# Optimization experiments

Hardware: AMD Instinct MI355X
Metric: run time of the kernel (lower is better)

## Reference

```python
import jax, jax.numpy as jnp
import numpy as np

# Mamba hyperparams (mamba_ssm defaults for d_model=128)
D_MODEL = 128
DEPTH = 8
D_INNER = 256   # expand=2
D_STATE = 16
D_CONV = 4
DT_RANK = 8     # ceil(D_MODEL/16)
EPS = 1e-5


def setup_inputs() -> dict:
    key = jax.random.key(0)
    ks = jax.random.split(key, 8)
    B, H, W = 1, 48, 48
    s = lambda k, shape, sc=0.02: jax.random.normal(k, shape, jnp.float32) * sc
    return {
        "x": jax.random.normal(ks[0], (B, D_MODEL, H, W), jnp.float32),
        "W_in": s(ks[1], (DEPTH, D_MODEL, 2 * D_INNER)),
        "conv_w": s(ks[2], (DEPTH, D_INNER, D_CONV), 0.2),
        "conv_b": jnp.zeros((DEPTH, D_INNER), jnp.float32),
        "W_xproj": s(ks[3], (DEPTH, D_INNER, DT_RANK + 2 * D_STATE)),
        "W_dt": s(ks[4], (DEPTH, DT_RANK, D_INNER), 0.1),
        "b_dt": jnp.full((DEPTH, D_INNER), -4.6, jnp.float32),  # softplus ~= 0.01
        "A_log": jnp.broadcast_to(
            jnp.log(jnp.arange(1, D_STATE + 1, dtype=jnp.float32)),
            (DEPTH, D_INNER, D_STATE)).copy(),
        "D_skip": jnp.ones((DEPTH, D_INNER), jnp.float32),
        "W_out": s(ks[5], (DEPTH, D_INNER, D_MODEL)),
        "rms_w": jnp.ones((DEPTH, D_MODEL), jnp.float32),
    }


def _rmsnorm(x, w):
    return x * jax.lax.rsqrt(jnp.mean(x * x, axis=-1, keepdims=True) + EPS) * w


def _mamba_layer(x, Wi, cw, cb, Wx, Wdt, bdt, Alog, Dp, Wo):
    # x: [B, L, D_MODEL]
    B, L, _ = x.shape
    xz = x @ Wi                                   # [B, L, 2*d_inner]
    xi, z = jnp.split(xz, 2, axis=-1)
    # causal depthwise conv1d, kernel D_CONV
    xp = jnp.pad(xi, ((0, 0), (D_CONV - 1, 0), (0, 0)))
    xc = sum(xp[:, k:k + L, :] * cw[:, k] for k in range(D_CONV)) + cb
    xc = jax.nn.silu(xc)                          # [B, L, d_inner]
    dbl = xc @ Wx                                 # [B, L, dt_rank + 2*d_state]
    dt_r = dbl[..., :DT_RANK]
    Bs = dbl[..., DT_RANK:DT_RANK + D_STATE]      # [B, L, d_state]
    Cs = dbl[..., DT_RANK + D_STATE:]
    dt = jax.nn.softplus(dt_r @ Wdt + bdt)        # [B, L, d_inner]
    A = -jnp.exp(Alog)                            # [d_inner, d_state]
    dA = jnp.exp(dt[..., None] * A)               # [B, L, d_inner, d_state]
    dBx = (dt * xc)[..., None] * Bs[:, :, None, :]
    # linear recurrence h_t = dA_t * h_{t-1} + dBx_t via parallel scan
    def comb(l, r):
        al, bl = l
        ar, br = r
        return ar * al, ar * bl + br
    _, h = jax.lax.associative_scan(comb, (dA, dBx), axis=1)
    y = jnp.einsum('blds,bls->bld', h, Cs) + Dp * xc
    y = y * jax.nn.silu(z)
    return y @ Wo                                 # [B, L, D_MODEL]


def reference(x, W_in, conv_w, conv_b, W_xproj, W_dt, b_dt, A_log, D_skip, W_out, rms_w):
    B, C, H, W = x.shape
    seq = x.reshape(B, C, H * W).transpose(0, 2, 1)  # [B, L, C]
    for l in range(DEPTH):
        seq = _mamba_layer(seq, W_in[l], conv_w[l], conv_b[l], W_xproj[l],
                           W_dt[l], b_dt[l], A_log[l], D_skip[l], W_out[l])
        seq = _rmsnorm(seq, rms_w[l])
    return seq.reshape(B, H, W, C).transpose(0, 3, 1, 2)
```

## Files before the change

kernel.cpp:

```cpp
#include <hip/hip_runtime.h>
#include <math.h>

#define LSEQ 2304
#define DM 128
#define DI 256
#define DS 16
#define RK 8
#define NCH 576
#define CLEN 4
#define NG 24
#define GS 24
#define NSI (DI*DS)
#define EPSF 1e-5f

__device__ __forceinline__ float silu_f(float s) { return s / (1.f + __expf(-s)); }
__device__ __forceinline__ float softplus_f(float x) { return (x > 20.f) ? x : log1pf(__expf(x)); }

template<bool FIRST>
__global__ __launch_bounds__(256, 4)
void k_in(const float* __restrict__ seq, const float* __restrict__ x0,
          const float* __restrict__ Wi,
          const float* __restrict__ cw, const float* __restrict__ cbias,
          float* __restrict__ xc_g, float* __restrict__ sz_g) {
    __shared__ float As[19 * 128];
    const int l0 = blockIdx.x * 16;
    const int half = blockIdx.y & 1;
    const bool isZ = blockIdx.y >= 2;
    const int tid = threadIdx.x;

    if (FIRST) {
        const int rlo = isZ ? 3 : 0;
        for (int idx = tid + rlo * 128; idx < 19 * 128; idx += 256) {
            const int r = idx >> 7, cc = idx & 127;
            const int l = l0 - 3 + r;
            As[idx] = (l >= 0) ? x0[cc * LSEQ + l] : 0.f;
        }
    } else if (!isZ) {
        for (int idx = tid; idx < 19 * 32; idx += 256) {
            const int r = idx >> 5, cq = (idx & 31) * 4;
            const int l = l0 - 3 + r;
            const float4 v = (l >= 0) ? *(const float4*)&seq[l * DM + cq]
                                      : make_float4(0.f, 0.f, 0.f, 0.f);
            *(float4*)&As[r * 128 + cq] = v;
        }
    } else {
        for (int idx = tid; idx < 16 * 32; idx += 256) {
            const int r = 3 + (idx >> 5), cq = (idx & 31) * 4;
            *(float4*)&As[r * 128 + cq] =
                *(const float4*)&seq[(l0 - 3 + r) * DM + cq];
        }
    }
    __syncthreads();

    const int c = tid & 127;
    const int rg = tid >> 7;
    const int d = half * 128 + c;

    if (!isZ) {
        float ax[11];
#pragma unroll
        for (int r = 0; r < 11; ++r) ax[r] = 0.f;
        for (int k4 = 0; k4 < 32; ++k4) {
            float bv[4];
#pragma unroll
            for (int u = 0; u < 4; ++u) bv[u] = Wi[(k4 * 4 + u) * 512 + d];
#pragma unroll
            for (int r = 0; r < 11; ++r) {
                const float4 a4 = *(const float4*)&As[(rg * 8 + r) * 128 + k4 * 4];
                ax[r] += a4.x * bv[0] + a4.y * bv[1] + a4.z * bv[2] + a4.w * bv[3];
            }
        }
        const float w0 = cw[d * 4 + 0], w1 = cw[d * 4 + 1];
        const float w2 = cw[d * 4 + 2], w3 = cw[d * 4 + 3];
        const float cbv = cbias[d];
#pragma unroll
        for (int rr = 0; rr < 8; ++rr) {
            const float v = silu_f(cbv + w0 * ax[rr] + w1 * ax[rr + 1] +
                                   w2 * ax[rr + 2] + w3 * ax[rr + 3]);
            xc_g[(l0 + rg * 8 + rr) * DI + d] = v;
        }
    } else {
        float az[8];
#pragma unroll
        for (int r = 0; r < 8; ++r) az[r] = 0.f;
        for (int k4 = 0; k4 < 32; ++k4) {
            float bv[4];
#pragma unroll
            for (int u = 0; u < 4; ++u) bv[u] = Wi[(k4 * 4 + u) * 512 + 256 + d];
#pragma unroll
            for (int r = 0; r < 8; ++r) {
                const float4 a4 = *(const float4*)&As[(rg * 8 + r + 3) * 128 + k4 * 4];
                az[r] += a4.x * bv[0] + a4.y * bv[1] + a4.z * bv[2] + a4.w * bv[3];
            }
        }
#pragma unroll
        for (int rr = 0; rr < 8; ++rr)
            sz_g[(l0 + rg * 8 + rr) * DI + d] = silu_f(az[rr]);
    }
}

__global__ __launch_bounds__(256, 4)
void k_mid2(const float* __restrict__ xc_g,
            const float* __restrict__ Wx,
            const float* __restrict__ Wdt, const float* __restrict__ bdt,
            const float* __restrict__ Alog,
            float* __restrict__ dbl_g, float* __restrict__ dt_g,
            float* __restrict__ P, float* __restrict__ S) {
    __shared__ float xcs[CLEN * 256];
    __shared__ float part[4 * 160];
    __shared__ float dtrs[CLEN * 8];
    __shared__ float dbls[CLEN * 32];
    const int c = blockIdx.x;
    const int l0 = c * CLEN;
    const int tid = threadIdx.x;
    const int d = tid;

    ((float4*)xcs)[tid] = ((const float4*)&xc_g[l0 * DI])[tid];
    __syncthreads();

    for (int task = tid; task < 640; task += 256) {
        const int kc = task / 160;
        const int o = task - kc * 160;
        const int r = o / 40, j = o - r * 40;
        const float* xr = &xcs[r * 256 + kc * 64];
        const float* wp = &Wx[(kc * 64) * 40 + j];
        float acc = 0.f;
#pragma unroll 8
        for (int k = 0; k < 64; ++k) acc += xr[k] * wp[k * 40];
        part[kc * 160 + o] = acc;
    }
    __syncthreads();
    if (tid < 160) {
        const float acc = part[tid] + part[160 + tid] + part[320 + tid] + part[480 + tid];
        const int r = tid / 40, j = tid - r * 40;
        if (j < RK) dtrs[r * 8 + j] = acc;
        else {
            dbls[r * 32 + (j - 8)] = acc;
            dbl_g[(l0 + r) * 32 + (j - 8)] = acc;
        }
    }
    __syncthreads();

    float dtv[CLEN], xcv[CLEN];
    {
        float wdt[8];
#pragma unroll
        for (int q = 0; q < 8; ++q) wdt[q] = Wdt[q * DI + d];
        const float bdv = bdt[d];
#pragma unroll
        for (int r = 0; r < CLEN; ++r) {
            float acc = bdv;
#pragma unroll
            for (int q = 0; q < 8; ++q) acc += dtrs[r * 8 + q] * wdt[q];
            dtv[r] = softplus_f(acc);
            dt_g[(l0 + r) * DI + d] = dtv[r];
            xcv[r] = xcs[r * 256 + d];
        }
    }

    float A[16], pr[16], hs[16];
#pragma unroll
    for (int v = 0; v < 4; ++v) {
        const float4 a4 = *(const float4*)&Alog[d * DS + v * 4];
        A[v * 4 + 0] = -__expf(a4.x);
        A[v * 4 + 1] = -__expf(a4.y);
        A[v * 4 + 2] = -__expf(a4.z);
        A[v * 4 + 3] = -__expf(a4.w);
    }
#pragma unroll
    for (int s = 0; s < 16; ++s) { pr[s] = 1.f; hs[s] = 0.f; }
#pragma unroll
    for (int t = 0; t < CLEN; ++t) {
        const float dtt = dtv[t];
        const float uv = dtt * xcv[t];
        const float* Brow = &dbls[t * 32];
#pragma unroll
        for (int s = 0; s < 16; ++s) {
            const float e = __expf(dtt * A[s]);
            pr[s] *= e;
            hs[s] = e * hs[s] + uv * Brow[s];
        }
    }
    const int base = c * NSI + d * DS;
#pragma unroll
    for (int v = 0; v < 4; ++v) {
        *(float4*)&P[base + v * 4] =
            make_float4(pr[v * 4], pr[v * 4 + 1], pr[v * 4 + 2], pr[v * 4 + 3]);
        *(float4*)&S[base + v * 4] =
            make_float4(hs[v * 4], hs[v * 4 + 1], hs[v * 4 + 2], hs[v * 4 + 3]);
    }
}

__global__ __launch_bounds__(256, 4)
void k_carry1(float* __restrict__ P, float* __restrict__ S,
              float* __restrict__ Pg, float* __restrict__ Sg) {
    const int g = blockIdx.x;
    const int i = blockIdx.y * 256 + threadIdx.x;
    float G = 0.f, Pp = 1.f;
    const int base = g * GS * NSI + i;
#pragma unroll 8
    for (int k = 0; k < GS; ++k) {
        const int idx = base + k * NSI;
        const float p = P[idx];
        const float s = S[idx];
        S[idx] = G;
        P[idx] = Pp;
        G = p * G + s;
        Pp *= p;
    }
    Pg[g * NSI + i] = Pp;
    Sg[g * NSI + i] = G;
}

__global__ __launch_bounds__(256, 4)
void k_carry2(const float* __restrict__ Pg, float* __restrict__ Sg) {
    const int i = blockIdx.x * 256 + threadIdx.x;
    float G = 0.f;
#pragma unroll 8
    for (int g = 0; g < NG; ++g) {
        const int idx = g * NSI + i;
        const float p = Pg[idx];
        const float s = Sg[idx];
        Sg[idx] = G;
        G = p * G + s;
    }
}

template<bool LAST>
__global__ __launch_bounds__(256, 3)
void k_tail(const float* __restrict__ dt_g, const float* __restrict__ xc_g,
            const float* __restrict__ dbl_g, const float* __restrict__ Alog,
            const float* __restrict__ Sloc, const float* __restrict__ Ppre,
            const float* __restrict__ Gc, const float* __restrict__ Dp,
            const float* __restrict__ sz_g, const float* __restrict__ Wo,
            const float* __restrict__ rmsw, float* __restrict__ seq,
            float* __restrict__ out) {
    __shared__ float dbls[CLEN * 32];
    __shared__ float Ys[CLEN * 256];
    __shared__ float partO[4 * CLEN * 128];
    __shared__ float Os[CLEN * 129];
    __shared__ float red[CLEN * 32];
    __shared__ float scaleS[CLEN];
    const int c = blockIdx.x;
    const int g = c / GS;
    const int l0 = c * CLEN;
    const int tid = threadIdx.x;
    const int d = tid;

    if (tid < CLEN * 32) dbls[tid] = dbl_g[l0 * 32 + tid];

    float A[16], h[16];
#pragma unroll
    for (int v = 0; v < 4; ++v) {
        const float4 a4 = *(const float4*)&Alog[d * DS + v * 4];
        A[v * 4 + 0] = -__expf(a4.x);
        A[v * 4 + 1] = -__expf(a4.y);
        A[v * 4 + 2] = -__expf(a4.z);
        A[v * 4 + 3] = -__expf(a4.w);
        const float4 s4 = *(const float4*)&Sloc[c * NSI + d * DS + v * 4];
        const float4 p4 = *(const float4*)&Ppre[c * NSI + d * DS + v * 4];
        const float4 g4 = *(const float4*)&Gc[g * NSI + d * DS + v * 4];
        h[v * 4 + 0] = s4.x + p4.x * g4.x;
        h[v * 4 + 1] = s4.y + p4.y * g4.y;
        h[v * 4 + 2] = s4.z + p4.z * g4.z;
        h[v * 4 + 3] = s4.w + p4.w * g4.w;
    }
    float dtv[CLEN], xcv[CLEN], szv[CLEN];
#pragma unroll
    for (int r = 0; r < CLEN; ++r) {
        dtv[r] = dt_g[(l0 + r) * DI + d];
        xcv[r] = xc_g[(l0 + r) * DI + d];
        szv[r] = sz_g[(l0 + r) * DI + d];
    }
    const float dskip = Dp[d];
    __syncthreads();
#pragma unroll
    for (int t = 0; t < CLEN; ++t) {
        const float dtt = dtv[t];
        const float uv = dtt * xcv[t];
        float sum = 0.f;
#pragma unroll
        for (int s = 0; s < 16; ++s) {
            const float e = __expf(dtt * A[s]);
            h[s] = e * h[s] + uv * dbls[t * 32 + s];
            sum += h[s] * dbls[t * 32 + 16 + s];
        }
        Ys[t * 256 + d] = (sum + dskip * xcv[t]) * szv[t];
    }
    __syncthreads();

    {
        const int ccp = tid & 63;
        const int kg = tid >> 6;
        float acc[CLEN][2];
#pragma unroll
        for (int r = 0; r < CLEN; ++r) { acc[r][0] = 0.f; acc[r][1] = 0.f; }
        const float* wp = &Wo[(kg * 64) * DM + ccp * 2];
        const float* yp = &Ys[kg * 64];
#pragma unroll 8
        for (int k = 0; k < 64; ++k) {
            const float2 w2 = *(const float2*)(wp + k * DM);
#pragma unroll
            for (int r = 0; r < CLEN; ++r) {
                const float yv = yp[r * 256 + k];
                acc[r][0] += yv * w2.x;
                acc[r][1] += yv * w2.y;
            }
        }
#pragma unroll
        for (int r = 0; r < CLEN; ++r) {
            partO[(kg * CLEN + r) * 128 + ccp * 2 + 0] = acc[r][0];
            partO[(kg * CLEN + r) * 128 + ccp * 2 + 1] = acc[r][1];
        }
        __syncthreads();
        for (int idx = tid; idx < CLEN * 128; idx += 256) {
            const int r = idx >> 7, cc = idx & 127;
            Os[r * 129 + cc] = partO[(0 * CLEN + r) * 128 + cc] +
                               partO[(1 * CLEN + r) * 128 + cc] +
                               partO[(2 * CLEN + r) * 128 + cc] +
                               partO[(3 * CLEN + r) * 128 + cc];
        }
        __syncthreads();
    }

    if (tid < CLEN * 32) {
        const int r = tid >> 5, part = tid & 31;
        float ss = 0.f;
#pragma unroll
        for (int i = 0; i < 4; ++i) {
            const float v = Os[r * 129 + part * 4 + i];
            ss += v * v;
        }
        red[tid] = ss;
    }
    __syncthreads();
    if (tid < CLEN) {
        float ss = 0.f;
#pragma unroll
        for (int p = 0; p < 32; ++p) ss += red[tid * 32 + p];
        scaleS[tid] = rsqrtf(ss * (1.f / DM) + EPSF);
    }
    __syncthreads();
    if (LAST) {
        for (int idx = tid; idx < CLEN * DM; idx += 256) {
            const int r = idx >> 7, cc = idx & 127;
            out[cc * LSEQ + (l0 + r)] = Os[r * 129 + cc] * scaleS[r] * rmsw[cc];
        }
    } else {
        for (int idx = tid; idx < CLEN * DM; idx += 256) {
            const int r = idx >> 7, cc = idx & 127;
            seq[(l0 + r) * DM + cc] = Os[r * 129 + cc] * scaleS[r] * rmsw[cc];
        }
    }
}

extern "C" void kernel_launch(void* const* d_in, const int* in_sizes, int n_in,
                              void* d_out, int out_size, void* d_ws, size_t ws_size,
                              hipStream_t stream) {
    const float* x    = (const float*)d_in[0];
    const float* W_in = (const float*)d_in[1];
    const float* cw   = (const float*)d_in[2];
    const float* cb   = (const float*)d_in[3];
    const float* Wx   = (const float*)d_in[4];
    const float* Wdt  = (const float*)d_in[5];
    const float* bdt  = (const float*)d_in[6];
    const float* Alog = (const float*)d_in[7];
    const float* Dp   = (const float*)d_in[8];
    const float* Wo   = (const float*)d_in[9];
    const float* rmsw = (const float*)d_in[10];
    float* out = (float*)d_out;

    float* ws   = (float*)d_ws;
    float* seq  = ws; ws += LSEQ * DM;
    float* szb  = ws; ws += LSEQ * DI;
    float* xcb  = ws; ws += LSEQ * DI;
    float* dtb  = ws; ws += LSEQ * DI;
    float* dblb = ws; ws += LSEQ * 32;
    float* Pb   = ws; ws += NCH * NSI;
    float* Sb   = ws; ws += NCH * NSI;
    float* Pgb  = ws; ws += NG * NSI;
    float* Sgb  = ws; ws += NG * NSI;

    for (int layer = 0; layer < 8; ++layer) {
        const float* Wi_l   = W_in + (size_t)layer * DM * 512;
        const float* cw_l   = cw   + (size_t)layer * DI * 4;
        const float* cb_l   = cb   + (size_t)layer * DI;
        const float* Wx_l   = Wx   + (size_t)layer * DI * 40;
        const float* Wdt_l  = Wdt  + (size_t)layer * RK * DI;
        const float* bdt_l  = bdt  + (size_t)layer * DI;
        const float* Alog_l = Alog + (size_t)layer * DI * DS;
        const float* Dp_l   = Dp   + (size_t)layer * DI;
        const float* Wo_l   = Wo   + (size_t)layer * DI * DM;
        const float* rmsw_l = rmsw + (size_t)layer * DM;

        if (layer == 0)
            k_in<true><<<dim3(144, 4), 256, 0, stream>>>(seq, x, Wi_l, cw_l, cb_l,
                                                         xcb, szb);
        else
            k_in<false><<<dim3(144, 4), 256, 0, stream>>>(seq, x, Wi_l, cw_l, cb_l,
                                                          xcb, szb);

        k_mid2<<<NCH, 256, 0, stream>>>(xcb, Wx_l, Wdt_l, bdt_l, Alog_l,
                                        dblb, dtb, Pb, Sb);

        k_carry1<<<dim3(NG, 16), 256, 0, stream>>>(Pb, Sb, Pgb, Sgb);
        k_carry2<<<16, 256, 0, stream>>>(Pgb, Sgb);

        if (layer == 7)
            k_tail<true><<<NCH, 256, 0, stream>>>(dtb, xcb, dblb, Alog_l, Sb, Pb,
                                                  Sgb, Dp_l, szb, Wo_l, rmsw_l,
                                                  seq, out);
        else
            k_tail<false><<<NCH, 256, 0, stream>>>(dtb, xcb, dblb, Alog_l, Sb, Pb,
                                                   Sgb, Dp_l, szb, Wo_l, rmsw_l,
                                                   seq, out);
    }
}
```

Before: 554.1 us.

## Replace stored decay products with per-chunk dt sums and recompute dt in tail

The per-state decay products P are no longer stored per chunk. Because the decay of each state is exp(A*sum(dt)), only a per-chunk dt sum per channel is written, and the carry kernel rebuilds the chunk and prefix decays from it with exp. The tail kernel also recomputes dt from the raw projection (dbl now keeps all 40 columns) instead of reading a stored dt buffer. The aim is to cut the large NCH*NSI P read/write traffic and the LSEQ*DI dt traffic, in exchange for extra exp and softplus work and slightly different rounding.

```diff
diff --git a/kernel.cpp b/kernel.cpp
--- a/kernel.cpp
+++ b/kernel.cpp
@@ -104,8 +104,8 @@
             const float* __restrict__ Wx,
             const float* __restrict__ Wdt, const float* __restrict__ bdt,
             const float* __restrict__ Alog,
-            float* __restrict__ dbl_g, float* __restrict__ dt_g,
-            float* __restrict__ P, float* __restrict__ S) {
+            float* __restrict__ dbl_g, float* __restrict__ dts_g,
+            float* __restrict__ S) {
     __shared__ float xcs[CLEN * 256];
     __shared__ float part[4 * 160];
     __shared__ float dtrs[CLEN * 8];
@@ -133,11 +133,9 @@
     if (tid < 160) {
         const float acc = part[tid] + part[160 + tid] + part[320 + tid] + part[480 + tid];
         const int r = tid / 40, j = tid - r * 40;
+        dbl_g[(l0 + r) * 40 + j] = acc;
         if (j < RK) dtrs[r * 8 + j] = acc;
-        else {
-            dbls[r * 32 + (j - 8)] = acc;
-            dbl_g[(l0 + r) * 32 + (j - 8)] = acc;
-        }
+        else dbls[r * 32 + (j - 8)] = acc;
     }
     __syncthreads();
 
@@ -153,12 +151,12 @@
 #pragma unroll
             for (int q = 0; q < 8; ++q) acc += dtrs[r * 8 + q] * wdt[q];
             dtv[r] = softplus_f(acc);
-            dt_g[(l0 + r) * DI + d] = dtv[r];
             xcv[r] = xcs[r * 256 + d];
         }
     }
-
-    float A[16], pr[16], hs[16];
+    dts_g[c * DI + d] = dtv[0] + dtv[1] + dtv[2] + dtv[3];
+
+    float A[16], hs[16];
 #pragma unroll
     for (int v = 0; v < 4; ++v) {
         const float4 a4 = *(const float4*)&Alog[d * DS + v * 4];
@@ -168,7 +166,7 @@
         A[v * 4 + 3] = -__expf(a4.w);
     }
 #pragma unroll
-    for (int s = 0; s < 16; ++s) { pr[s] = 1.f; hs[s] = 0.f; }
+    for (int s = 0; s < 16; ++s) hs[s] = 0.f;
 #pragma unroll
     for (int t = 0; t < CLEN; ++t) {
         const float dtt = dtv[t];
@@ -177,38 +175,41 @@
 #pragma unroll
         for (int s = 0; s < 16; ++s) {
             const float e = __expf(dtt * A[s]);
-            pr[s] *= e;
             hs[s] = e * hs[s] + uv * Brow[s];
         }
     }
     const int base = c * NSI + d * DS;
 #pragma unroll
     for (int v = 0; v < 4; ++v) {
-        *(float4*)&P[base + v * 4] =
-            make_float4(pr[v * 4], pr[v * 4 + 1], pr[v * 4 + 2], pr[v * 4 + 3]);
         *(float4*)&S[base + v * 4] =
             make_float4(hs[v * 4], hs[v * 4 + 1], hs[v * 4 + 2], hs[v * 4 + 3]);
     }
 }
 
 __global__ __launch_bounds__(256, 4)
-void k_carry1(float* __restrict__ P, float* __restrict__ S,
+void k_carry1(float* __restrict__ S, const float* __restrict__ dts,
+              const float* __restrict__ Alog,
+              float* __restrict__ dtspre,
               float* __restrict__ Pg, float* __restrict__ Sg) {
     const int g = blockIdx.x;
     const int i = blockIdx.y * 256 + threadIdx.x;
-    float G = 0.f, Pp = 1.f;
+    const int d = i >> 4;
+    const float Av = -__expf(Alog[i]);
+    float G = 0.f, cd = 0.f;
     const int base = g * GS * NSI + i;
+    const int c0 = g * GS;
 #pragma unroll 8
     for (int k = 0; k < GS; ++k) {
         const int idx = base + k * NSI;
-        const float p = P[idx];
+        const float dtsv = dts[(c0 + k) * DI + d];
+        if ((i & 15) == 0) dtspre[(c0 + k) * DI + d] = cd;
+        const float p = __expf(Av * dtsv);
         const float s = S[idx];
         S[idx] = G;
-        P[idx] = Pp;
         G = p * G + s;
-        Pp *= p;
-    }
-    Pg[g * NSI + i] = Pp;
+        cd += dtsv;
+    }
+    Pg[g * NSI + i] = __expf(Av * cd);
     Sg[g * NSI + i] = G;
 }
 
@@ -228,14 +229,14 @@
 
 template<bool LAST>
 __global__ __launch_bounds__(256, 3)
-void k_tail(const float* __restrict__ dt_g, const float* __restrict__ xc_g,
-            const float* __restrict__ dbl_g, const float* __restrict__ Alog,
-            const float* __restrict__ Sloc, const float* __restrict__ Ppre,
-            const float* __restrict__ Gc, const float* __restrict__ Dp,
-            const float* __restrict__ sz_g, const float* __restrict__ Wo,
-            const float* __restrict__ rmsw, float* __restrict__ seq,
-            float* __restrict__ out) {
-    __shared__ float dbls[CLEN * 32];
+void k_tail(const float* __restrict__ xc_g, const float* __restrict__ dbl_g,
+            const float* __restrict__ Alog, const float* __restrict__ Sloc,
+            const float* __restrict__ dtspre, const float* __restrict__ Gc,
+            const float* __restrict__ Dp, const float* __restrict__ sz_g,
+            const float* __restrict__ Wdt, const float* __restrict__ bdt,
+            const float* __restrict__ Wo, const float* __restrict__ rmsw,
+            float* __restrict__ seq, float* __restrict__ out) {
+    __shared__ float dbls[CLEN * 40];
     __shared__ float Ys[CLEN * 256];
     __shared__ float partO[4 * CLEN * 128];
     __shared__ float Os[CLEN * 129];
@@ -247,9 +248,10 @@
     const int tid = threadIdx.x;
     const int d = tid;
 
-    if (tid < CLEN * 32) dbls[tid] = dbl_g[l0 * 32 + tid];
+    if (tid < CLEN * 40) dbls[tid] = dbl_g[l0 * 40 + tid];
 
     float A[16], h[16];
+    const float cdts = dtspre[c * DI + d];
 #pragma unroll
     for (int v = 0; v < 4; ++v) {
         const float4 a4 = *(const float4*)&Alog[d * DS + v * 4];
@@ -258,32 +260,47 @@
         A[v * 4 + 2] = -__expf(a4.z);
         A[v * 4 + 3] = -__expf(a4.w);
         const float4 s4 = *(const float4*)&Sloc[c * NSI + d * DS + v * 4];
-        const float4 p4 = *(const float4*)&Ppre[c * NSI + d * DS + v * 4];
         const float4 g4 = *(const float4*)&Gc[g * NSI + d * DS + v * 4];
-        h[v * 4 + 0] = s4.x + p4.x * g4.x;
-        h[v * 4 + 1] = s4.y + p4.y * g4.y;
-        h[v * 4 + 2] = s4.z + p4.z * g4.z;
-        h[v * 4 + 3] = s4.w + p4.w * g4.w;
-    }
-    float dtv[CLEN], xcv[CLEN], szv[CLEN];
+        h[v * 4 + 0] = s4.x + __expf(A[v * 4 + 0] * cdts) * g4.x;
+        h[v * 4 + 1] = s4.y + __expf(A[v * 4 + 1] * cdts) * g4.y;
+        h[v * 4 + 2] = s4.z + __expf(A[v * 4 + 2] * cdts) * g4.z;
+        h[v * 4 + 3] = s4.w + __expf(A[v * 4 + 3] * cdts) * g4.w;
+    }
+    float xcv[CLEN], szv[CLEN];
 #pragma unroll
     for (int r = 0; r < CLEN; ++r) {
-        dtv[r] = dt_g[(l0 + r) * DI + d];
         xcv[r] = xc_g[(l0 + r) * DI + d];
         szv[r] = sz_g[(l0 + r) * DI + d];
     }
     const float dskip = Dp[d];
     __syncthreads();
+
+    float dtv[CLEN];
+    {
+        float wdt[8];
+#pragma unroll
+        for (int q = 0; q < 8; ++q) wdt[q] = Wdt[q * DI + d];
+        const float bdv = bdt[d];
+#pragma unroll
+        for (int r = 0; r < CLEN; ++r) {
+            float acc = bdv;
+#pragma unroll
+            for (int q = 0; q < 8; ++q) acc += dbls[r * 40 + q] * wdt[q];
+            dtv[r] = softplus_f(acc);
+        }
+    }
 #pragma unroll
     for (int t = 0; t < CLEN; ++t) {
         const float dtt = dtv[t];
         const float uv = dtt * xcv[t];
+        const float* Brow = &dbls[t * 40 + 8];
+        const float* Crow = &dbls[t * 40 + 24];
         float sum = 0.f;
 #pragma unroll
         for (int s = 0; s < 16; ++s) {
             const float e = __expf(dtt * A[s]);
-            h[s] = e * h[s] + uv * dbls[t * 32 + s];
-            sum += h[s] * dbls[t * 32 + 16 + s];
+            h[s] = e * h[s] + uv * Brow[s];
+            sum += h[s] * Crow[s];
         }
         Ys[t * 256 + d] = (sum + dskip * xcv[t]) * szv[t];
     }
@@ -370,16 +387,16 @@
     const float* rmsw = (const float*)d_in[10];
     float* out = (float*)d_out;
 
-    float* ws   = (float*)d_ws;
-    float* seq  = ws; ws += LSEQ * DM;
-    float* szb  = ws; ws += LSEQ * DI;
-    float* xcb  = ws; ws += LSEQ * DI;
-    float* dtb  = ws; ws += LSEQ * DI;
-    float* dblb = ws; ws += LSEQ * 32;
-    float* Pb   = ws; ws += NCH * NSI;
-    float* Sb   = ws; ws += NCH * NSI;
-    float* Pgb  = ws; ws += NG * NSI;
-    float* Sgb  = ws; ws += NG * NSI;
+    float* ws      = (float*)d_ws;
+    float* seq     = ws; ws += LSEQ * DM;
+    float* szb     = ws; ws += LSEQ * DI;
+    float* xcb     = ws; ws += LSEQ * DI;
+    float* dblb    = ws; ws += LSEQ * 40;
+    float* dtsb    = ws; ws += NCH * DI;
+    float* dtspreb = ws; ws += NCH * DI;
+    float* Sb      = ws; ws += NCH * NSI;
+    float* Pgb     = ws; ws += NG * NSI;
+    float* Sgb     = ws; ws += NG * NSI;
 
     for (int layer = 0; layer < 8; ++layer) {
         const float* Wi_l   = W_in + (size_t)layer * DM * 512;
@@ -401,18 +418,19 @@
                                                           xcb, szb);
 
         k_mid2<<<NCH, 256, 0, stream>>>(xcb, Wx_l, Wdt_l, bdt_l, Alog_l,
-                                        dblb, dtb, Pb, Sb);
-
-        k_carry1<<<dim3(NG, 16), 256, 0, stream>>>(Pb, Sb, Pgb, Sgb);
+                                        dblb, dtsb, Sb);
+
+        k_carry1<<<dim3(NG, 16), 256, 0, stream>>>(Sb, dtsb, Alog_l,
+                                                   dtspreb, Pgb, Sgb);
         k_carry2<<<16, 256, 0, stream>>>(Pgb, Sgb);
 
         if (layer == 7)
-            k_tail<true><<<NCH, 256, 0, stream>>>(dtb, xcb, dblb, Alog_l, Sb, Pb,
-                                                  Sgb, Dp_l, szb, Wo_l, rmsw_l,
-                                                  seq, out);
+            k_tail<true><<<NCH, 256, 0, stream>>>(xcb, dblb, Alog_l, Sb, dtspreb,
+                                                  Sgb, Dp_l, szb, Wdt_l, bdt_l,
+                                                  Wo_l, rmsw_l, seq, out);
         else
-            k_tail<false><<<NCH, 256, 0, stream>>>(dtb, xcb, dblb, Alog_l, Sb, Pb,
-                                                   Sgb, Dp_l, szb, Wo_l, rmsw_l,
-                                                   seq, out);
-    }
-}
+            k_tail<false><<<NCH, 256, 0, stream>>>(xcb, dblb, Alog_l, Sb, dtspreb,
+                                                   Sgb, Dp_l, szb, Wdt_l, bdt_l,
+                                                   Wo_l, rmsw_l, seq, out);
+    }
+}
```

New measurement: 574.8 us. 1.04x slower.

## Fuse carry kernels via last-block atomic counter; vectorize k_tail out-projection loads

Applied to the files above, without the earlier changes.

Merges the two carry-propagation kernels into one: each block increments a global atomic counter after writing its group totals, and the last block to finish runs the cross-group scan itself with float4 accesses. This removes one kernel launch per layer, eight in total. The cost is that the whole 4096-element group scan now runs in a single block of 256 threads, which is serialized work on one CU. Separately, the k_tail output-projection loop now loads four y values at once as float4 and four weight rows per iteration, to raise instruction-level parallelism.

```diff
diff --git a/kernel.cpp b/kernel.cpp
--- a/kernel.cpp
+++ b/kernel.cpp
@@ -21,12 +21,16 @@
 void k_in(const float* __restrict__ seq, const float* __restrict__ x0,
           const float* __restrict__ Wi,
           const float* __restrict__ cw, const float* __restrict__ cbias,
-          float* __restrict__ xc_g, float* __restrict__ sz_g) {
+          float* __restrict__ xc_g, float* __restrict__ sz_g,
+          int* __restrict__ counter) {
     __shared__ float As[19 * 128];
     const int l0 = blockIdx.x * 16;
     const int half = blockIdx.y & 1;
     const bool isZ = blockIdx.y >= 2;
     const int tid = threadIdx.x;
+
+    if (FIRST && blockIdx.x == 0 && blockIdx.y == 0 && tid == 0)
+        *counter = 0;
 
     if (FIRST) {
         const int rlo = isZ ? 3 : 0;
@@ -192,10 +196,13 @@
 }
 
 __global__ __launch_bounds__(256, 4)
-void k_carry1(float* __restrict__ P, float* __restrict__ S,
-              float* __restrict__ Pg, float* __restrict__ Sg) {
+void k_carry12(float* __restrict__ P, float* __restrict__ S,
+               float* __restrict__ Pg, float* __restrict__ Sg,
+               int* __restrict__ counter) {
+    __shared__ int lastFlag;
     const int g = blockIdx.x;
     const int i = blockIdx.y * 256 + threadIdx.x;
+    const int tid = threadIdx.x;
     float G = 0.f, Pp = 1.f;
     const int base = g * GS * NSI + i;
 #pragma unroll 8
@@ -210,19 +217,35 @@
     }
     Pg[g * NSI + i] = Pp;
     Sg[g * NSI + i] = G;
-}
-
-__global__ __launch_bounds__(256, 4)
-void k_carry2(const float* __restrict__ Pg, float* __restrict__ Sg) {
-    const int i = blockIdx.x * 256 + threadIdx.x;
-    float G = 0.f;
-#pragma unroll 8
-    for (int g = 0; g < NG; ++g) {
-        const int idx = g * NSI + i;
-        const float p = Pg[idx];
-        const float s = Sg[idx];
-        Sg[idx] = G;
-        G = p * G + s;
+
+    __threadfence();
+    __syncthreads();
+    if (tid == 0)
+        lastFlag = (atomicAdd(counter, 1) == NG * 16 - 1) ? 1 : 0;
+    __syncthreads();
+    if (lastFlag) {
+        __threadfence();
+        const int i0 = tid * 16;
+        float4 Gc[4];
+#pragma unroll
+        for (int v = 0; v < 4; ++v) Gc[v] = make_float4(0.f, 0.f, 0.f, 0.f);
+        for (int gg = 0; gg < NG; ++gg) {
+            const int b2 = gg * NSI + i0;
+#pragma unroll
+            for (int v = 0; v < 4; ++v) {
+                const float4 p4 = *(const float4*)&Pg[b2 + v * 4];
+                const float4 s4 = *(const float4*)&Sg[b2 + v * 4];
+                const float4 old = Gc[v];
+                *(float4*)&Sg[b2 + v * 4] = old;
+                Gc[v].x = p4.x * old.x + s4.x;
+                Gc[v].y = p4.y * old.y + s4.y;
+                Gc[v].z = p4.z * old.z + s4.z;
+                Gc[v].w = p4.w * old.w + s4.w;
+            }
+        }
+        __threadfence();
+        __syncthreads();
+        if (tid == 0) atomicExch(counter, 0);
     }
 }
 
@@ -297,14 +320,31 @@
         for (int r = 0; r < CLEN; ++r) { acc[r][0] = 0.f; acc[r][1] = 0.f; }
         const float* wp = &Wo[(kg * 64) * DM + ccp * 2];
         const float* yp = &Ys[kg * 64];
-#pragma unroll 8
-        for (int k = 0; k < 64; ++k) {
-            const float2 w2 = *(const float2*)(wp + k * DM);
+#pragma unroll 4
+        for (int k4 = 0; k4 < 16; ++k4) {
+            const float2 w0 = *(const float2*)(wp + (k4 * 4 + 0) * DM);
+            const float2 w1 = *(const float2*)(wp + (k4 * 4 + 1) * DM);
+            const float2 w2 = *(const float2*)(wp + (k4 * 4 + 2) * DM);
+            const float2 w3 = *(const float2*)(wp + (k4 * 4 + 3) * DM);
+            float4 y4[CLEN];
+#pragma unroll
+            for (int r = 0; r < CLEN; ++r)
+                y4[r] = *(const float4*)&yp[r * 256 + k4 * 4];
 #pragma unroll
             for (int r = 0; r < CLEN; ++r) {
-                const float yv = yp[r * 256 + k];
-                acc[r][0] += yv * w2.x;
-                acc[r][1] += yv * w2.y;
+                acc[r][0] += y4[r].x * w0.x; acc[r][1] += y4[r].x * w0.y;
+            }
+#pragma unroll
+            for (int r = 0; r < CLEN; ++r) {
+                acc[r][0] += y4[r].y * w1.x; acc[r][1] += y4[r].y * w1.y;
+            }
+#pragma unroll
+            for (int r = 0; r < CLEN; ++r) {
+                acc[r][0] += y4[r].z * w2.x; acc[r][1] += y4[r].z * w2.y;
+            }
+#pragma unroll
+            for (int r = 0; r < CLEN; ++r) {
+                acc[r][0] += y4[r].w * w3.x; acc[r][1] += y4[r].w * w3.y;
             }
         }
 #pragma unroll
@@ -380,6 +420,7 @@
     float* Sb   = ws; ws += NCH * NSI;
     float* Pgb  = ws; ws += NG * NSI;
     float* Sgb  = ws; ws += NG * NSI;
+    int*   cnt  = (int*)ws;
 
     for (int layer = 0; layer < 8; ++layer) {
         const float* Wi_l   = W_in + (size_t)layer * DM * 512;
@@ -395,16 +436,15 @@
 
         if (layer == 0)
             k_in<true><<<dim3(144, 4), 256, 0, stream>>>(seq, x, Wi_l, cw_l, cb_l,
-                                                         xcb, szb);
+                                                         xcb, szb, cnt);
         else
             k_in<false><<<dim3(144, 4), 256, 0, stream>>>(seq, x, Wi_l, cw_l, cb_l,
-                                                          xcb, szb);
+                                                          xcb, szb, cnt);
 
         k_mid2<<<NCH, 256, 0, stream>>>(xcb, Wx_l, Wdt_l, bdt_l, Alog_l,
                                         dblb, dtb, Pb, Sb);
 
-        k_carry1<<<dim3(NG, 16), 256, 0, stream>>>(Pb, Sb, Pgb, Sgb);
-        k_carry2<<<16, 256, 0, stream>>>(Pgb, Sgb);
+        k_carry12<<<dim3(NG, 16), 256, 0, stream>>>(Pb, Sb, Pgb, Sgb, cnt);
 
         if (layer == 7)
             k_tail<true><<<NCH, 256, 0, stream>>>(dtb, xcb, dblb, Alog_l, Sb, Pb,
```

Result: slower. 1.188 ms (+114.4%).
